# Kernel tuning notes

Measured on AMD Instinct MI355X. Metric: run time of the kernel, lower is better.

The kernel has to match this reference:

```python
import jax, jax.numpy as jnp
import numpy as np

NVAR, B, C, H, W = 3, 4, 256, 64, 64
C1 = C // 2          # dat channels (nc)
C2 = C - C1
HEADS = 4
HC = C1 // HEADS     # head channels
STRIDE = 4
KS = 4
HK, WK = H // STRIDE, W // STRIDE
NS = HK * WK         # n_sample
RPE_H, RPE_W = 2 * H - 1, 2 * W - 1
NPAIR = 3


def _grid_sample(img, grid):
    # img [B,C,Hi,Wi]; grid [B,Hg,Wg,2] = (x,y) in [-1,1]; bilinear, align_corners=True, zero-pad
    Bn, Cn, Hi, Wi = img.shape
    x = (grid[..., 0] + 1.0) * 0.5 * (Wi - 1)
    y = (grid[..., 1] + 1.0) * 0.5 * (Hi - 1)
    x0 = jnp.floor(x)
    y0 = jnp.floor(y)
    wx = x - x0
    wy = y - y0
    x0i = x0.astype(jnp.int32)
    y0i = y0.astype(jnp.int32)
    imt = img.transpose(0, 2, 3, 1)  # [B,Hi,Wi,C]
    bidx = jnp.arange(Bn)[:, None, None]

    def corner(yi, xi, wgt):
        ok = ((xi >= 0) & (xi < Wi) & (yi >= 0) & (yi < Hi)).astype(img.dtype)
        val = imt[bidx, jnp.clip(yi, 0, Hi - 1), jnp.clip(xi, 0, Wi - 1)]  # [B,Hg,Wg,C]
        return val * (wgt * ok)[..., None]

    out = (corner(y0i, x0i, (1 - wx) * (1 - wy))
           + corner(y0i, x0i + 1, wx * (1 - wy))
           + corner(y0i + 1, x0i, (1 - wx) * wy)
           + corner(y0i + 1, x0i + 1, wx * wy))
    return out.transpose(0, 3, 1, 2)  # [B,C,Hg,Wg]


def _ref_points(hk, wk):
    # normalized sampling-grid reference points, (y,x) order
    ry = (jnp.linspace(0.5, hk - 0.5, hk) / (hk - 1.0)) * 2.0 - 1.0
    rx = (jnp.linspace(0.5, wk - 0.5, wk) / (wk - 1.0)) * 2.0 - 1.0
    return jnp.stack(jnp.meshgrid(ry, rx, indexing='ij'), axis=-1)  # [hk,wk,2]


def _q_grid(h, w):
    gy = (jnp.arange(h, dtype=jnp.float32) / (h - 1.0)) * 2.0 - 1.0
    gx = (jnp.arange(w, dtype=jnp.float32) / (w - 1.0)) * 2.0 - 1.0
    return jnp.stack(jnp.meshgrid(gy, gx, indexing='ij'), axis=-1).reshape(h * w, 2)


def _conv1x1(x, w, b=None):
    y = jnp.einsum('oc,bchw->bohw', w, x)
    return y if b is None else y + b[None, :, None, None]


def _dat_block(q_in, kv_in, pWq, pbq, pWk, pbk, pWv, pbv, pWo, pbo,
               pdw_w, pdw_b, pln_g, pln_b, ppw_w, prpe):
    Bn = q_in.shape[0]
    q = _conv1x1(q_in, pWq, pbq)  # [B,C1,H,W]
    # offset net: depthwise 4x4 stride-4 conv -> channel LN -> GELU -> 1x1 conv to 2
    off = jax.lax.conv_general_dilated(
        q, pdw_w, (STRIDE, STRIDE), 'VALID',
        dimension_numbers=('NCHW', 'OIHW', 'NCHW'),
        feature_group_count=C1) + pdw_b[None, :, None, None]  # [B,C1,HK,WK]
    mu = off.mean(axis=1, keepdims=True)
    var = ((off - mu) ** 2).mean(axis=1, keepdims=True)
    off = (off - mu) * jax.lax.rsqrt(var + 1e-5) * pln_g[None, :, None, None] + pln_b[None, :, None, None]
    off = jax.nn.gelu(off, approximate=False)
    offset = _conv1x1(off, ppw_w).transpose(0, 2, 3, 1)  # [B,HK,WK,2] (dy,dx)
    # offset_range_factor = -1 -> no tanh scaling, clamp pos into [-1,1]
    pos = jnp.clip(offset + _ref_points(HK, WK)[None], -1.0, 1.0)  # [B,HK,WK,2]
    xs = _grid_sample(kv_in, pos[..., ::-1])  # sample kv at deformed points -> [B,C1,HK,WK]
    k = _conv1x1(xs, pWk, pbk).reshape(Bn, HEADS, HC, NS)
    v = _conv1x1(xs, pWv, pbv).reshape(Bn, HEADS, HC, NS)
    qh = q.reshape(Bn, HEADS, HC, H * W)
    attn = jnp.einsum('bhcm,bhcn->bhmn', qh, k) * (HC ** -0.5)  # [B,h,HW,NS]
    # relative position bias sampled from rpe table
    disp = (_q_grid(H, W)[None, :, None, :] - pos.reshape(Bn, 1, NS, 2)) * 0.5  # [B,HW,NS,2]
    rpe_b = jnp.broadcast_to(prpe[None], (Bn, HEADS, RPE_H, RPE_W))
    bias = _grid_sample(rpe_b, disp[..., ::-1])  # [B,h,HW,NS]
    attn = jax.nn.softmax(attn + bias, axis=-1)
    out = jnp.einsum('bhmn,bhcn->bhcm', attn, v).reshape(Bn, C1, H, W)
    return _conv1x1(out, pWo, pbo)


def _forward(xs, params):
    results = []
    num = 0
    for i in range(NVAR):
        res = xs[i]
        for j in range(i):
            attn_out = _dat_block(xs[i][:, :C1], xs[j][:, :C1],
                                  *(p[num] for p in params))
            # torch: res -= -cat(zeros[:,:C2], attn)  => add attn on channels C2:
            res = res.at[:, C2:].add(attn_out)
            num += 1
        results.append(res)
    return jnp.stack(results)  # [NVAR,B,C,H,W]


def setup_inputs() -> dict:
    key = jax.random.key(0)
    ks = jax.random.split(key, 4)
    d = {}
    for n, k in zip(['x0', 'x1', 'x2'], jax.random.split(ks[0], 3)):
        d[n] = jax.random.normal(k, (B, C, H, W), jnp.float32)

    def w(k, shape, s=0.02):
        return jax.random.normal(k, shape, jnp.float32) * s

    kk = jax.random.split(ks[1], 8)
    d['Wq'] = w(kk[0], (NPAIR, C1, C1))
    d['bq'] = jnp.zeros((NPAIR, C1), jnp.float32)
    d['Wk'] = w(kk[1], (NPAIR, C1, C1))
    d['bk'] = jnp.zeros((NPAIR, C1), jnp.float32)
    d['Wv'] = w(kk[2], (NPAIR, C1, C1))
    d['bv'] = jnp.zeros((NPAIR, C1), jnp.float32)
    d['Wo'] = w(kk[3], (NPAIR, C1, C1))
    d['bo'] = jnp.zeros((NPAIR, C1), jnp.float32)
    d['dw_w'] = w(kk[4], (NPAIR, C1, 1, KS, KS), 0.1)
    d['dw_b'] = jnp.zeros((NPAIR, C1), jnp.float32)
    d['ln_g'] = jnp.ones((NPAIR, C1), jnp.float32)
    d['ln_b'] = jnp.zeros((NPAIR, C1), jnp.float32)
    d['pw_w'] = w(kk[5], (NPAIR, 2, C1), 0.1)
    d['rpe'] = w(kk[6], (NPAIR, HEADS, RPE_H, RPE_W), 0.01)
    return d


def reference(x0, x1, x2, Wq, bq, Wk, bk, Wv, bv, Wo, bo,
              dw_w, dw_b, ln_g, ln_b, pw_w, rpe):
    params = (Wq, bq, Wk, bk, Wv, bv, Wo, bo, dw_w, dw_b, ln_g, ln_b, pw_w, rpe)
    out = _forward([x0, x1, x2], params)
    flow = jnp.zeros((NVAR, x0.shape[0]), out.dtype)
    return out, flow
```

## Files before the change

kernel.cpp:

```cpp
#include <hip/hip_runtime.h>
#include <math.h>

#define NVAR 3
#define BB 4
#define CC 256
#define C1 128
#define HEADS 4
#define HH 64
#define WW 64
#define HW 4096
#define RPE_W 127
#define NP 3
#define SCALE 0.17677669529663687f

typedef short bf16x8 __attribute__((ext_vector_type(8)));
typedef float f32x4 __attribute__((ext_vector_type(4)));
typedef __bf16 bf16x2 __attribute__((ext_vector_type(2)));

__device__ __forceinline__ unsigned short f2bf(float f) {
    unsigned int u = __float_as_uint(f);
    u += 0x7fffu + ((u >> 16) & 1u);
    return (unsigned short)(u >> 16);
}
__device__ __forceinline__ float bflo(unsigned u) { return __uint_as_float(u << 16); }
__device__ __forceinline__ float bfhi(unsigned u) { return __uint_as_float(u & 0xffff0000u); }

__device__ __forceinline__ float dot2bf(unsigned a, unsigned b, float c) {
#if __has_builtin(__builtin_amdgcn_fdot2_f32_bf16)
    return __builtin_amdgcn_fdot2_f32_bf16(__builtin_bit_cast(bf16x2, a),
                                           __builtin_bit_cast(bf16x2, b), c, false);
#else
    return c + bflo(a) * bflo(b) + bfhi(a) * bfhi(b);
#endif
}

__global__ __launch_bounds__(256) void prep_copy(const float* __restrict__ rpe,
                                                 const float* __restrict__ Wq,
                                                 const float* __restrict__ Wo,
                                                 const float* __restrict__ Wk,
                                                 const float* __restrict__ Wv,
                                                 const float* __restrict__ x0,
                                                 unsigned short* __restrict__ tabbf,
                                                 unsigned short* __restrict__ wqh,
                                                 unsigned short* __restrict__ wql,
                                                 unsigned short* __restrict__ woh,
                                                 unsigned short* __restrict__ wkh,
                                                 unsigned short* __restrict__ wvh,
                                                 float* __restrict__ out) {
    int blk = blockIdx.x;
    if (blk >= 24) {
        const long long n4 = (long long)BB * CC * HW / 4;
        long long i = (long long)(blk - 24) * 256 + threadIdx.x;
        const long long stride = 1024LL * 256;
        for (; i < n4 + 12; i += stride) {
            if (i < n4) ((float4*)out)[i] = ((const float4*)x0)[i];
            else out[3LL * BB * CC * HW + (i - n4)] = 0.f;
        }
        return;
    }
    if (blk < 12) {
        const float* src = rpe + (long long)blk * RPE_W * RPE_W;
        unsigned short* dst = tabbf + (long long)blk * 16384;
        for (int idx = threadIdx.x; idx < 16384; idx += 256) {
            int y = idx >> 7, x = idx & 127;
            float v = (y < RPE_W && x < RPE_W) ? src[y * RPE_W + x] : 0.f;
            dst[idx] = f2bf(v);
        }
    } else if (blk < 15) {
        int p = blk - 12;
        for (int i = threadIdx.x; i < 16384; i += 256) {
            float w = Wq[p * 16384 + i];
            unsigned short h = f2bf(w);
            wqh[p * 16384 + i] = h;
            wql[p * 16384 + i] = f2bf(w - bflo((unsigned)h));
        }
    } else if (blk < 18) {
        int p = blk - 15;
        for (int i = threadIdx.x; i < 16384; i += 256)
            woh[p * 16384 + i] = f2bf(Wo[p * 16384 + i]);
    } else if (blk < 21) {
        int p = blk - 18;
        for (int i = threadIdx.x; i < 16384; i += 256)
            wkh[p * 16384 + i] = f2bf(Wk[p * 16384 + i]);
    } else {
        int p = blk - 21;
        for (int i = threadIdx.x; i < 16384; i += 256)
            wvh[p * 16384 + i] = f2bf(Wv[p * 16384 + i]);
    }
}

__global__ __launch_bounds__(256) void conv_q(const float* __restrict__ x1,
                                              const float* __restrict__ x2,
                                              const unsigned short* __restrict__ wqh,
                                              const unsigned short* __restrict__ wql,
                                              const float* __restrict__ bq,
                                              float* __restrict__ qbuf,
                                              unsigned short* __restrict__ qbf,
                                              float* __restrict__ out) {
    __shared__ unsigned short qlds[4][16][136];
    int wid = threadIdx.x >> 6, lane = threadIdx.x & 63;
    int g = lane >> 4, lm = lane & 15;
    int gw = blockIdx.x * 4 + wid;
    int mt = gw & 255;
    int pb = gw >> 8;
    int p = pb >> 2, b = pb & 3;
    const float* X = ((p == 0) ? x1 : x2) + (long long)b * CC * HW;
    int m = mt * 16 + lm;
    float* outc = (p < 2)
        ? out + (((long long)((p + 1) * 4 + b)) * CC) * HW + m
        : nullptr;

    bf16x8 bhi[4], blo[4];
#pragma unroll
    for (int ksl = 0; ksl < 4; ksl++) {
        float v[8];
#pragma unroll
        for (int j = 0; j < 8; j++) {
            int k = ksl * 32 + 8 * g + j;
            v[j] = X[(long long)k * HW + m];
            if (outc) outc[(long long)k * HW] = v[j];
        }
        union { unsigned u[4]; bf16x8 v; } H, L;
#pragma unroll
        for (int t = 0; t < 4; t++) {
            unsigned short h0 = f2bf(v[2 * t]), h1 = f2bf(v[2 * t + 1]);
            unsigned short l0 = f2bf(v[2 * t] - bflo((unsigned)h0));
            unsigned short l1 = f2bf(v[2 * t + 1] - bflo((unsigned)h1));
            H.u[t] = (unsigned)h0 | ((unsigned)h1 << 16);
            L.u[t] = (unsigned)l0 | ((unsigned)l1 << 16);
        }
        bhi[ksl] = H.v;
        blo[ksl] = L.v;
    }

    const unsigned short* WH = wqh + p * 16384;
    const unsigned short* WL = wql + p * 16384;
    unsigned short* ql = &qlds[wid][lm][0];
    f32x4 zero = {0.f, 0.f, 0.f, 0.f};
#pragma unroll
    for (int ct2 = 0; ct2 < 4; ct2++) {
        int ct0 = 2 * ct2, ct1 = ct0 + 1;
        f32x4 a0 = zero, a1 = zero;
#pragma unroll
        for (int ksl = 0; ksl < 4; ksl++) {
            bf16x8 Ah0 = *(const bf16x8*)(WH + (ct0 * 16 + lm) * 128 + ksl * 32 + 8 * g);
            bf16x8 Al0 = *(const bf16x8*)(WL + (ct0 * 16 + lm) * 128 + ksl * 32 + 8 * g);
            bf16x8 Ah1 = *(const bf16x8*)(WH + (ct1 * 16 + lm) * 128 + ksl * 32 + 8 * g);
            bf16x8 Al1 = *(const bf16x8*)(WL + (ct1 * 16 + lm) * 128 + ksl * 32 + 8 * g);
            a0 = __builtin_amdgcn_mfma_f32_16x16x32_bf16(Ah0, bhi[ksl], a0, 0, 0, 0);
            a1 = __builtin_amdgcn_mfma_f32_16x16x32_bf16(Ah1, bhi[ksl], a1, 0, 0, 0);
            a0 = __builtin_amdgcn_mfma_f32_16x16x32_bf16(Ah0, blo[ksl], a0, 0, 0, 0);
            a1 = __builtin_amdgcn_mfma_f32_16x16x32_bf16(Ah1, blo[ksl], a1, 0, 0, 0);
            a0 = __builtin_amdgcn_mfma_f32_16x16x32_bf16(Al0, bhi[ksl], a0, 0, 0, 0);
            a1 = __builtin_amdgcn_mfma_f32_16x16x32_bf16(Al1, bhi[ksl], a1, 0, 0, 0);
        }
        float q0[4], q1[4];
#pragma unroll
        for (int r = 0; r < 4; r++) {
            int c0 = ct0 * 16 + 4 * g + r, c1 = ct1 * 16 + 4 * g + r;
            q0[r] = a0[r] + bq[p * 128 + c0];
            q1[r] = a1[r] + bq[p * 128 + c1];
            qbuf[((long long)pb * 128 + c0) * HW + m] = q0[r];
            qbuf[((long long)pb * 128 + c1) * HW + m] = q1[r];
        }
        *(unsigned*)(ql + ct0 * 16 + 4 * g) =
            (unsigned)f2bf(q0[0] * SCALE) | ((unsigned)f2bf(q0[1] * SCALE) << 16);
        *(unsigned*)(ql + ct0 * 16 + 4 * g + 2) =
            (unsigned)f2bf(q0[2] * SCALE) | ((unsigned)f2bf(q0[3] * SCALE) << 16);
        *(unsigned*)(ql + ct1 * 16 + 4 * g) =
            (unsigned)f2bf(q1[0] * SCALE) | ((unsigned)f2bf(q1[1] * SCALE) << 16);
        *(unsigned*)(ql + ct1 * 16 + 4 * g + 2) =
            (unsigned)f2bf(q1[2] * SCALE) | ((unsigned)f2bf(q1[3] * SCALE) << 16);
    }

    unsigned short* Yb = qbf + ((long long)pb * HW + mt * 16) * 128;
    int q = lane >> 4, cg = lane & 15;
#pragma unroll
    for (int i = 0; i < 4; i++) {
        int row = i * 4 + q;
        uint4 vv = *(const uint4*)&qlds[wid][row][cg * 8];
        *(uint4*)(Yb + row * 128 + cg * 8) = vv;
    }
}

__global__ __launch_bounds__(256) void mid_kernel(const float* __restrict__ qbuf,
                                                  const float* __restrict__ dw_w,
                                                  const float* __restrict__ dw_b,
                                                  const float* __restrict__ ln_g,
                                                  const float* __restrict__ ln_b,
                                                  const float* __restrict__ pw_w,
                                                  const float* __restrict__ x0,
                                                  const float* __restrict__ x1,
                                                  float* __restrict__ posb,
                                                  uint4* __restrict__ prmb,
                                                  unsigned short* __restrict__ xT) {
    __shared__ float sm[32 * 4 * 65 + 16 * 128];
    int blk = blockIdx.x;
    int tid = threadIdx.x;
    if (blk < 192) {
        float (*ld)[4][65] = (float(*)[4][65])sm;
        float (*dwout)[128] = (float(*)[128])(sm + 32 * 4 * 65);
        int pb = blk >> 4, hk = blk & 15;
        int p = pb >> 2;
        for (int cq = 0; cq < 4; cq++) {
            int c32 = cq * 32;
            __syncthreads();
#pragma unroll
            for (int it = 0; it < 8; it++) {
                int i2 = tid + it * 256;
                int c = i2 >> 6, rem = i2 & 63;
                int y = rem >> 4, xq = rem & 15;
                float4 v = *(const float4*)(qbuf + ((long long)pb * 128 + c32 + c) * HW
                                            + (4 * hk + y) * 64 + xq * 4);
                ld[c][y][xq * 4 + 0] = v.x;
                ld[c][y][xq * 4 + 1] = v.y;
                ld[c][y][xq * 4 + 2] = v.z;
                ld[c][y][xq * 4 + 3] = v.w;
            }
            __syncthreads();
            int wk = tid >> 4;
#pragma unroll
            for (int oi = 0; oi < 2; oi++) {
                int c = (tid & 15) + oi * 16;
                const float* dwp = dw_w + (p * 128 + c32 + c) * 16;
                float acc = dw_b[p * 128 + c32 + c];
#pragma unroll
                for (int ky = 0; ky < 4; ky++)
#pragma unroll
                    for (int kx = 0; kx < 4; kx++)
                        acc += ld[c][ky][wk * 4 + kx] * dwp[ky * 4 + kx];
                dwout[wk][c32 + c] = acc;
            }
        }
        __syncthreads();
        int wid = tid >> 6, lane = tid & 63;
        for (int i = 0; i < 4; i++) {
            int wk = wid * 4 + i;
            int s = hk * 16 + wk;
            float a0 = dwout[wk][lane], a1 = dwout[wk][lane + 64];
            float s1 = a0 + a1;
#pragma unroll
            for (int o = 1; o < 64; o <<= 1) s1 += __shfl_xor(s1, o);
            float mu = s1 * (1.f / 128.f);
            float d0 = a0 - mu, d1 = a1 - mu;
            float v2 = d0 * d0 + d1 * d1;
#pragma unroll
            for (int o = 1; o < 64; o <<= 1) v2 += __shfl_xor(v2, o);
            float rs = rsqrtf(v2 * (1.f / 128.f) + 1e-5f);
            int c0 = lane, c1 = lane + 64;
            float y0 = d0 * rs * ln_g[p * 128 + c0] + ln_b[p * 128 + c0];
            float y1 = d1 * rs * ln_g[p * 128 + c1] + ln_b[p * 128 + c1];
            float g0 = 0.5f * y0 * (1.f + erff(y0 * 0.70710678118654752f));
            float g1 = 0.5f * y1 * (1.f + erff(y1 * 0.70710678118654752f));
            float o0 = pw_w[(p * 2 + 0) * 128 + c0] * g0
                     + pw_w[(p * 2 + 0) * 128 + c1] * g1;
            float o1 = pw_w[(p * 2 + 1) * 128 + c0] * g0
                     + pw_w[(p * 2 + 1) * 128 + c1] * g1;
#pragma unroll
            for (int o = 1; o < 64; o <<= 1) o0 += __shfl_xor(o0, o);
#pragma unroll
            for (int o = 1; o < 64; o <<= 1) o1 += __shfl_xor(o1, o);
            if (lane == 0) {
                int wk2 = s & 15;
                float refy = (hk + 0.5f) * (2.f / 15.f) - 1.f;
                float refx = (wk2 + 0.5f) * (2.f / 15.f) - 1.f;
                float py = fminf(fmaxf(o0 + refy, -1.f), 1.f);
                float px = fminf(fmaxf(o1 + refx, -1.f), 1.f);
                int pbn = pb * 256 + s;
                posb[pbn * 2 + 0] = py;
                posb[pbn * 2 + 1] = px;
                float cy = 31.5f * (1.f - py), cx = 31.5f * (1.f - px);
                float yf = floorf(cy), xf = floorf(cx);
                float wy = cy - yf, wx = cx - xf;
                int Y0 = (int)yf, X0 = (int)xf;
                uint4 v;
                v.x = (unsigned)f2bf((1.f - wy) * (1.f - wx))
                    | ((unsigned)f2bf((1.f - wy) * wx) << 16);
                v.y = (unsigned)f2bf(wy * (1.f - wx))
                    | ((unsigned)f2bf(wy * wx) << 16);
                v.z = (unsigned)((Y0 * 128 + X0) * 2);
                v.w = 0;
                prmb[pbn] = v;
            }
        }
    } else {
        float (*ld2)[65] = (float(*)[65])sm;
        int rem = blk - 192;
        int v = rem >> 10;
        int rem1 = rem & 1023;
        int b = rem1 >> 8;
        int rem2 = rem1 & 255;
        int ct = rem2 >> 6;
        int mt = rem2 & 63;
        const float* src = ((v == 0) ? x0 : x1) + (long long)b * CC * HW
                           + (long long)(ct * 32) * HW + mt * 64;
#pragma unroll
        for (int it = 0; it < 2; it++) {
            int c = tid >> 3, x4 = (tid & 7) + it * 8;
            float4 w = *(const float4*)(src + (long long)c * HW + x4 * 4);
            ld2[c][x4 * 4 + 0] = w.x;
            ld2[c][x4 * 4 + 1] = w.y;
            ld2[c][x4 * 4 + 2] = w.z;
            ld2[c][x4 * 4 + 3] = w.w;
        }
        __syncthreads();
        int m = tid >> 2, cg = tid & 3;
        union { unsigned u[4]; } pk;
#pragma unroll
        for (int t = 0; t < 4; t++) {
            unsigned short h0 = f2bf(ld2[cg * 8 + 2 * t][m]);
            unsigned short h1 = f2bf(ld2[cg * 8 + 2 * t + 1][m]);
            pk.u[t] = (unsigned)h0 | ((unsigned)h1 << 16);
        }
        *(uint4*)(xT + (((long long)(v * 4 + b)) * HW + mt * 64 + m) * 128
                  + ct * 32 + cg * 8) = *(uint4*)pk.u;
    }
}

__global__ __launch_bounds__(256) void sample_kv(const unsigned short* __restrict__ xT,
                                                 const float* __restrict__ posb,
                                                 const unsigned short* __restrict__ wkh,
                                                 const unsigned short* __restrict__ wvh,
                                                 const float* __restrict__ bk,
                                                 const float* __restrict__ bv,
                                                 unsigned short* __restrict__ kbf,
                                                 unsigned short* __restrict__ vbf) {
    __shared__ unsigned short xls[32 * 128];
    int blk = blockIdx.x;
    int pb = blk >> 3;
    int nt = blk & 7;
    int p = pb >> 2, b = pb & 3;
    int n0 = nt * 32;
    int tid = threadIdx.x;

    {
        int nl = tid >> 3, co = tid & 7;
        int n = n0 + nl;
        float py = posb[(pb * 256 + n) * 2 + 0];
        float px = posb[(pb * 256 + n) * 2 + 1];
        float yi = (py + 1.f) * 31.5f, xi = (px + 1.f) * 31.5f;
        yi = fminf(fmaxf(yi, 0.f), 63.f);
        xi = fminf(fmaxf(xi, 0.f), 63.f);
        int y0 = min((int)yi, 62);
        int x0i = min((int)xi, 62);
        float wy = yi - (float)y0, wx = xi - (float)x0i;
        float w00 = (1.f - wy) * (1.f - wx), w01 = (1.f - wy) * wx;
        float w10 = wy * (1.f - wx), w11 = wy * wx;
        int vsel = (p == 2) ? 1 : 0;
        const unsigned short* base = xT + ((long long)(vsel * 4 + b)) * HW * 128;
        int m00 = y0 * 64 + x0i;
        char* dst = (char*)xls;
#pragma unroll
        for (int cb = 0; cb < 2; cb++) {
            int c0 = co * 16 + cb * 8;
            bf16x8 a = *(const bf16x8*)(base + (long long)m00 * 128 + c0);
            bf16x8 bb = *(const bf16x8*)(base + (long long)(m00 + 1) * 128 + c0);
            bf16x8 cc = *(const bf16x8*)(base + (long long)(m00 + 64) * 128 + c0);
            bf16x8 dd = *(const bf16x8*)(base + (long long)(m00 + 65) * 128 + c0);
            union { unsigned u[4]; bf16x8 v; } R;
#pragma unroll
            for (int t = 0; t < 4; t++) {
                float r0 = w00 * bflo((unsigned)(unsigned short)a[2 * t])
                         + w01 * bflo((unsigned)(unsigned short)bb[2 * t])
                         + w10 * bflo((unsigned)(unsigned short)cc[2 * t])
                         + w11 * bflo((unsigned)(unsigned short)dd[2 * t]);
                float r1 = w00 * bflo((unsigned)(unsigned short)a[2 * t + 1])
                         + w01 * bflo((unsigned)(unsigned short)bb[2 * t + 1])
                         + w10 * bflo((unsigned)(unsigned short)cc[2 * t + 1])
                         + w11 * bflo((unsigned)(unsigned short)dd[2 * t + 1]);
                R.u[t] = (unsigned)f2bf(r0) | ((unsigned)f2bf(r1) << 16);
            }
            *(bf16x8*)(dst + ((nl * 256 + c0 * 2) ^ ((nl & 7) << 4))) = R.v;
        }
    }
    __syncthreads();

    int wid = tid >> 6, lane = tid & 63;
    int g = lane >> 4, lm = lane & 15;
    int ntile = wid & 1, isv = wid >> 1;
    int nl = ntile * 16 + lm;
    const char* srcl = (const char*)xls;
    bf16x8 xf[4];
#pragma unroll
    for (int ks = 0; ks < 4; ks++)
        xf[ks] = *(const bf16x8*)(srcl + ((nl * 256 + (ks * 32 + 8 * g) * 2)
                                          ^ ((nl & 7) << 4)));
    f32x4 zero = {0.f, 0.f, 0.f, 0.f};
    if (!isv) {
        const unsigned short* WK = wkh + p * 16384;
#pragma unroll
        for (int ct = 0; ct < 8; ct++) {
            f32x4 acc = zero;
#pragma unroll
            for (int ks = 0; ks < 4; ks++) {
                bf16x8 wf = *(const bf16x8*)(WK + (ct * 16 + lm) * 128 + ks * 32 + 8 * g);
                acc = __builtin_amdgcn_mfma_f32_16x16x32_bf16(xf[ks], wf, acc, 0, 0, 0);
            }
            float bias = bk[p * 128 + ct * 16 + lm];
#pragma unroll
            for (int r = 0; r < 4; r++) {
                int n = n0 + ntile * 16 + 4 * g + r;
                kbf[((long long)pb * 256 + n) * 128 + ct * 16 + lm] = f2bf(acc[r] + bias);
            }
        }
    } else {
        const unsigned short* WV = wvh + p * 16384;
#pragma unroll
        for (int ct = 0; ct < 8; ct++) {
            f32x4 acc = zero;
#pragma unroll
            for (int ks = 0; ks < 4; ks++) {
                bf16x8 wf = *(const bf16x8*)(WV + (ct * 16 + lm) * 128 + ks * 32 + 8 * g);
                acc = __builtin_amdgcn_mfma_f32_16x16x32_bf16(wf, xf[ks], acc, 0, 0, 0);
            }
#pragma unroll
            for (int r = 0; r < 4; r++) {
                int c = ct * 16 + 4 * g + r;
                vbf[((long long)pb * 128 + c) * 256 + n0 + ntile * 16 + lm]
                    = f2bf(acc[r] + bv[p * 128 + c]);
            }
        }
    }
}

__global__ __launch_bounds__(512, 4) void attn_mfma(
        const unsigned short* __restrict__ qbf,
        const unsigned short* __restrict__ kbf,
        const unsigned short* __restrict__ vbf,
        const unsigned short* __restrict__ tabbf,
        const uint4* __restrict__ prmb,
        float* __restrict__ obuf) {
    __shared__ unsigned short tab[16384 + 8];
    __shared__ uint4 prm[256];
    int tid = threadIdx.x;
    int wid = tid >> 6, lane = tid & 63;
    int g = lane >> 4, lm = lane & 15;
    int bid = blockIdx.x;
    int my = ((bid & 31) << 1) + (wid >> 2);
    int h = (bid >> 5) & 3;
    int b = (bid >> 7) & 3;
    int p = bid >> 9;
    int pb = p * 4 + b;

    {
        const uint4* ts = (const uint4*)(tabbf + (long long)(p * 4 + h) * 16384);
        uint4* td = (uint4*)tab;
#pragma unroll
        for (int i = 0; i < 4; i++) td[tid + i * 512] = ts[tid + i * 512];
        if (tid < 256) prm[tid] = prmb[pb * 256 + tid];
    }
    __syncthreads();

    int mx = ((wid & 3) << 4) + lm;

    bf16x8 qf = *(const bf16x8*)(qbf + ((long long)pb * HW + my * 64 + mx) * 128
                                 + h * 32 + 8 * g);
    const unsigned short* kbase = kbf + ((long long)pb * 256 + lm) * 128
                                  + h * 32 + 8 * g;
    f32x4 zero = {0.f, 0.f, 0.f, 0.f};
    f32x4 acc[16];
    __builtin_amdgcn_s_setprio(1);
#pragma unroll
    for (int ni = 0; ni < 16; ni++) {
        bf16x8 kf = *(const bf16x8*)(kbase + ni * 16 * 128);
        acc[ni] = __builtin_amdgcn_mfma_f32_16x16x32_bf16(kf, qf, zero, 0, 0, 0);
    }
    __builtin_amdgcn_s_setprio(0);

    int laneoff = (my * 128 + mx) * 2;
    const char* tb = (const char*)tab;
#pragma unroll
    for (int ni = 0; ni < 16; ni++) {
#pragma unroll
        for (int r = 0; r < 4; r++) {
            int n = ni * 16 + 4 * g + r;
            uint4 pw = prm[n];
            int va = (int)pw.z + laneoff;
            int va4 = va & ~3;
            int sh = va & 3;
            unsigned r0 = *(const unsigned*)(tb + va4);
            unsigned r1 = *(const unsigned*)(tb + va4 + 4);
            unsigned r2 = *(const unsigned*)(tb + va4 + 256);
            unsigned r3 = *(const unsigned*)(tb + va4 + 260);
            unsigned p0 = __builtin_amdgcn_alignbyte(r1, r0, sh);
            unsigned p1 = __builtin_amdgcn_alignbyte(r3, r2, sh);
            float t = acc[ni][r];
            t = dot2bf(p0, pw.x, t);
            t = dot2bf(p1, pw.y, t);
            acc[ni][r] = t;
        }
    }

    float mxv = -1e30f;
#pragma unroll
    for (int ni = 0; ni < 16; ni++)
        mxv = fmaxf(mxv, fmaxf(fmaxf(acc[ni][0], acc[ni][1]),
                               fmaxf(acc[ni][2], acc[ni][3])));
    mxv = fmaxf(mxv, __shfl_xor(mxv, 16));
    mxv = fmaxf(mxv, __shfl_xor(mxv, 32));
    float sum = 0.f;
    unsigned dwA[16], dwB[16];
#pragma unroll
    for (int ni = 0; ni < 16; ni++) {
        float e0 = __expf(acc[ni][0] - mxv);
        float e1 = __expf(acc[ni][1] - mxv);
        float e2 = __expf(acc[ni][2] - mxv);
        float e3 = __expf(acc[ni][3] - mxv);
        sum += (e0 + e1) + (e2 + e3);
        asm("v_cvt_pk_bf16_f32 %0, %1, %2" : "=v"(dwA[ni]) : "v"(e0), "v"(e1));
        asm("v_cvt_pk_bf16_f32 %0, %1, %2" : "=v"(dwB[ni]) : "v"(e2), "v"(e3));
    }
    sum += __shfl_xor(sum, 16);
    sum += __shfl_xor(sum, 32);

    int src0 = ((g & 1) << 5) + lm;
    int src1 = src0 + 16;
    bool sel = (g >> 1) != 0;
    const unsigned short* vb0 = vbf + ((long long)pb * 128 + h * 32 + lm) * 256
                                + 8 * g;
    f32x4 o0 = zero, o1 = zero;
#pragma unroll
    for (int st = 0; st < 8; st++) {
        unsigned d0a = __shfl(dwA[2 * st], src0), d0b = __shfl(dwA[2 * st + 1], src0);
        unsigned d1a = __shfl(dwB[2 * st], src0), d1b = __shfl(dwB[2 * st + 1], src0);
        unsigned d2a = __shfl(dwA[2 * st], src1), d2b = __shfl(dwA[2 * st + 1], src1);
        unsigned d3a = __shfl(dwB[2 * st], src1), d3b = __shfl(dwB[2 * st + 1], src1);
        union { unsigned u[4]; bf16x8 v; } pf;
        pf.u[0] = sel ? d0b : d0a;
        pf.u[1] = sel ? d1b : d1a;
        pf.u[2] = sel ? d2b : d2a;
        pf.u[3] = sel ? d3b : d3a;
        bf16x8 v0 = *(const bf16x8*)(vb0 + st * 32);
        bf16x8 v1 = *(const bf16x8*)(vb0 + 4096 + st * 32);
        __builtin_amdgcn_s_setprio(1);
        o0 = __builtin_amdgcn_mfma_f32_16x16x32_bf16(v0, pf.v, o0, 0, 0, 0);
        o1 = __builtin_amdgcn_mfma_f32_16x16x32_bf16(v1, pf.v, o1, 0, 0, 0);
        __builtin_amdgcn_s_setprio(0);
    }

    float inv = 1.f / sum;
    float* ob = obuf + ((long long)pb * 128 + h * 32) * HW + my * 64 + mx;
#pragma unroll
    for (int r = 0; r < 4; r++) {
        ob[(g * 4 + r) * HW] = o0[r] * inv;
        ob[(16 + g * 4 + r) * HW] = o1[r] * inv;
    }
}

__global__ __launch_bounds__(256) void conv_wo(const float* __restrict__ x1,
                                               const float* __restrict__ x2,
                                               const float* __restrict__ obuf,
                                               const unsigned short* __restrict__ woh,
                                               const float* __restrict__ bo,
                                               float* __restrict__ out) {
    int wid = threadIdx.x >> 6, lane = threadIdx.x & 63;
    int g = lane >> 4, lm = lane & 15;
    int gw = blockIdx.x * 4 + wid;
    int mt = gw & 255;
    int b = (gw >> 8) & 3;
    int vs = gw >> 10;
    int m = mt * 16 + lm;
    int np = vs + 1;

    f32x4 acc[8];
#pragma unroll
    for (int ct = 0; ct < 8; ct++) acc[ct] = (f32x4){0.f, 0.f, 0.f, 0.f};

    for (int pi = 0; pi < np; pi++) {
        int p = vs ? (1 + pi) : 0;
        const float* O = obuf + (long long)(p * 4 + b) * 128 * HW;
        bf16x8 bh[4];
#pragma unroll
        for (int ksl = 0; ksl < 4; ksl++) {
            float v[8];
#pragma unroll
            for (int j = 0; j < 8; j++)
                v[j] = O[(long long)(ksl * 32 + 8 * g + j) * HW + m];
            union { unsigned u[4]; bf16x8 v; } H;
#pragma unroll
            for (int t = 0; t < 4; t++)
                H.u[t] = (unsigned)f2bf(v[2 * t]) | ((unsigned)f2bf(v[2 * t + 1]) << 16);
            bh[ksl] = H.v;
        }
        const unsigned short* WH = woh + p * 16384;
#pragma unroll
        for (int ct = 0; ct < 8; ct++)
#pragma unroll
            for (int ksl = 0; ksl < 4; ksl++) {
                bf16x8 A = *(const bf16x8*)(WH + (ct * 16 + lm) * 128 + ksl * 32 + 8 * g);
                acc[ct] = __builtin_amdgcn_mfma_f32_16x16x32_bf16(A, bh[ksl], acc[ct], 0, 0, 0);
            }
    }

    int qi = vs + 1;
    const float* xq = (vs ? x2 : x1) + (long long)b * CC * HW;
#pragma unroll
    for (int ct = 0; ct < 8; ct++)
#pragma unroll
        for (int r = 0; r < 4; r++) {
            int c = ct * 16 + 4 * g + r;
            float bias = vs ? (bo[128 + c] + bo[256 + c]) : bo[c];
            float base = xq[(long long)(128 + c) * HW + m];
            out[(((long long)(qi * 4 + b)) * CC + 128 + c) * HW + m]
                = base + acc[ct][r] + bias;
        }
}

extern "C" void kernel_launch(void* const* d_in, const int* in_sizes, int n_in,
                              void* d_out, int out_size, void* d_ws, size_t ws_size,
                              hipStream_t stream) {
    const float* x0 = (const float*)d_in[0];
    const float* x1 = (const float*)d_in[1];
    const float* x2 = (const float*)d_in[2];
    const float* Wq = (const float*)d_in[3];
    const float* bq = (const float*)d_in[4];
    const float* Wk = (const float*)d_in[5];
    const float* bk = (const float*)d_in[6];
    const float* Wv = (const float*)d_in[7];
    const float* bv = (const float*)d_in[8];
    const float* Wo = (const float*)d_in[9];
    const float* bo = (const float*)d_in[10];
    const float* dw_w = (const float*)d_in[11];
    const float* dw_b = (const float*)d_in[12];
    const float* ln_g = (const float*)d_in[13];
    const float* ln_b = (const float*)d_in[14];
    const float* pw_w = (const float*)d_in[15];
    const float* rpe = (const float*)d_in[16];
    float* out = (float*)d_out;

    float* ws = (float*)d_ws;
    float* qbuf = ws;
    float* obuf = qbuf;
    float* posb = ws + 6291456;
    unsigned short* xT = (unsigned short*)(posb + 6144);
    unsigned short* qbf = xT + 4194304;
    unsigned short* kbf = qbf + 12582912;
    unsigned short* vbf = kbf + 393216;
    unsigned short* tabbf = vbf + 393216;
    uint4* prmb = (uint4*)(tabbf + 196608);
    unsigned short* wqh = (unsigned short*)(prmb + 3072);
    unsigned short* wql = wqh + 49152;
    unsigned short* woh = wql + 49152;
    unsigned short* wkh = woh + 49152;
    unsigned short* wvh = wkh + 49152;

    prep_copy<<<1048, 256, 0, stream>>>(rpe, Wq, Wo, Wk, Wv, x0, tabbf,
                                        wqh, wql, woh, wkh, wvh, out);
    conv_q<<<768, 256, 0, stream>>>(x1, x2, wqh, wql, bq, qbuf, qbf, out);
    mid_kernel<<<2240, 256, 0, stream>>>(qbuf, dw_w, dw_b, ln_g, ln_b, pw_w,
                                         x0, x1, posb, prmb, xT);
    sample_kv<<<96, 256, 0, stream>>>(xT, posb, wkh, wvh, bk, bv, kbf, vbf);
    attn_mfma<<<1536, 512, 0, stream>>>(qbf, kbf, vbf, tabbf, prmb, obuf);
    conv_wo<<<512, 256, 0, stream>>>(x1, x2, obuf, woh, bo, out);
}
```

Measured before the change: 181.1 us.

## Use online softmax over two key chunks and read RPE table from global

```diff
diff --git a/kernel.cpp b/kernel.cpp
--- a/kernel.cpp
+++ b/kernel.cpp
@@ -423,122 +423,130 @@
     }
 }
 
-__global__ __launch_bounds__(512, 4) void attn_mfma(
+__global__ __launch_bounds__(256, 4) void attn_mfma(
         const unsigned short* __restrict__ qbf,
         const unsigned short* __restrict__ kbf,
         const unsigned short* __restrict__ vbf,
         const unsigned short* __restrict__ tabbf,
         const uint4* __restrict__ prmb,
         float* __restrict__ obuf) {
-    __shared__ unsigned short tab[16384 + 8];
     __shared__ uint4 prm[256];
     int tid = threadIdx.x;
     int wid = tid >> 6, lane = tid & 63;
     int g = lane >> 4, lm = lane & 15;
     int bid = blockIdx.x;
-    int my = ((bid & 31) << 1) + (wid >> 2);
-    int h = (bid >> 5) & 3;
-    int b = (bid >> 7) & 3;
-    int p = bid >> 9;
+    int my = bid & 63;
+    int h = (bid >> 6) & 3;
+    int b = (bid >> 8) & 3;
+    int p = bid >> 10;
     int pb = p * 4 + b;
 
-    {
-        const uint4* ts = (const uint4*)(tabbf + (long long)(p * 4 + h) * 16384);
-        uint4* td = (uint4*)tab;
-#pragma unroll
-        for (int i = 0; i < 4; i++) td[tid + i * 512] = ts[tid + i * 512];
-        if (tid < 256) prm[tid] = prmb[pb * 256 + tid];
-    }
+    prm[tid] = prmb[pb * 256 + tid];
     __syncthreads();
 
-    int mx = ((wid & 3) << 4) + lm;
+    int mx = (wid << 4) + lm;
 
     bf16x8 qf = *(const bf16x8*)(qbf + ((long long)pb * HW + my * 64 + mx) * 128
                                  + h * 32 + 8 * g);
     const unsigned short* kbase = kbf + ((long long)pb * 256 + lm) * 128
                                   + h * 32 + 8 * g;
+    const char* tbg = (const char*)(tabbf + (long long)(p * 4 + h) * 16384);
+    const unsigned short* vb0 = vbf + ((long long)pb * 128 + h * 32 + lm) * 256
+                                + 8 * g;
+    int laneoff = (my * 128 + mx) * 2;
+
     f32x4 zero = {0.f, 0.f, 0.f, 0.f};
-    f32x4 acc[16];
-    __builtin_amdgcn_s_setprio(1);
-#pragma unroll
-    for (int ni = 0; ni < 16; ni++) {
-        bf16x8 kf = *(const bf16x8*)(kbase + ni * 16 * 128);
-        acc[ni] = __builtin_amdgcn_mfma_f32_16x16x32_bf16(kf, qf, zero, 0, 0, 0);
-    }
-    __builtin_amdgcn_s_setprio(0);
-
-    int laneoff = (my * 128 + mx) * 2;
-    const char* tb = (const char*)tab;
-#pragma unroll
-    for (int ni = 0; ni < 16; ni++) {
-#pragma unroll
-        for (int r = 0; r < 4; r++) {
-            int n = ni * 16 + 4 * g + r;
-            uint4 pw = prm[n];
-            int va = (int)pw.z + laneoff;
-            int va4 = va & ~3;
-            int sh = va & 3;
-            unsigned r0 = *(const unsigned*)(tb + va4);
-            unsigned r1 = *(const unsigned*)(tb + va4 + 4);
-            unsigned r2 = *(const unsigned*)(tb + va4 + 256);
-            unsigned r3 = *(const unsigned*)(tb + va4 + 260);
-            unsigned p0 = __builtin_amdgcn_alignbyte(r1, r0, sh);
-            unsigned p1 = __builtin_amdgcn_alignbyte(r3, r2, sh);
-            float t = acc[ni][r];
-            t = dot2bf(p0, pw.x, t);
-            t = dot2bf(p1, pw.y, t);
-            acc[ni][r] = t;
-        }
-    }
-
-    float mxv = -1e30f;
-#pragma unroll
-    for (int ni = 0; ni < 16; ni++)
-        mxv = fmaxf(mxv, fmaxf(fmaxf(acc[ni][0], acc[ni][1]),
-                               fmaxf(acc[ni][2], acc[ni][3])));
-    mxv = fmaxf(mxv, __shfl_xor(mxv, 16));
-    mxv = fmaxf(mxv, __shfl_xor(mxv, 32));
-    float sum = 0.f;
-    unsigned dwA[16], dwB[16];
-#pragma unroll
-    for (int ni = 0; ni < 16; ni++) {
-        float e0 = __expf(acc[ni][0] - mxv);
-        float e1 = __expf(acc[ni][1] - mxv);
-        float e2 = __expf(acc[ni][2] - mxv);
-        float e3 = __expf(acc[ni][3] - mxv);
-        sum += (e0 + e1) + (e2 + e3);
-        asm("v_cvt_pk_bf16_f32 %0, %1, %2" : "=v"(dwA[ni]) : "v"(e0), "v"(e1));
-        asm("v_cvt_pk_bf16_f32 %0, %1, %2" : "=v"(dwB[ni]) : "v"(e2), "v"(e3));
-    }
-    sum += __shfl_xor(sum, 16);
-    sum += __shfl_xor(sum, 32);
-
+    f32x4 o0 = zero, o1 = zero;
+    float m_run = -1e30f, l_run = 0.f;
     int src0 = ((g & 1) << 5) + lm;
     int src1 = src0 + 16;
     bool sel = (g >> 1) != 0;
-    const unsigned short* vb0 = vbf + ((long long)pb * 128 + h * 32 + lm) * 256
-                                + 8 * g;
-    f32x4 o0 = zero, o1 = zero;
-#pragma unroll
-    for (int st = 0; st < 8; st++) {
-        unsigned d0a = __shfl(dwA[2 * st], src0), d0b = __shfl(dwA[2 * st + 1], src0);
-        unsigned d1a = __shfl(dwB[2 * st], src0), d1b = __shfl(dwB[2 * st + 1], src0);
-        unsigned d2a = __shfl(dwA[2 * st], src1), d2b = __shfl(dwA[2 * st + 1], src1);
-        unsigned d3a = __shfl(dwB[2 * st], src1), d3b = __shfl(dwB[2 * st + 1], src1);
-        union { unsigned u[4]; bf16x8 v; } pf;
-        pf.u[0] = sel ? d0b : d0a;
-        pf.u[1] = sel ? d1b : d1a;
-        pf.u[2] = sel ? d2b : d2a;
-        pf.u[3] = sel ? d3b : d3a;
-        bf16x8 v0 = *(const bf16x8*)(vb0 + st * 32);
-        bf16x8 v1 = *(const bf16x8*)(vb0 + 4096 + st * 32);
+
+#pragma unroll
+    for (int ch = 0; ch < 2; ch++) {
+        int nb = ch * 128;
+        f32x4 acc[8];
         __builtin_amdgcn_s_setprio(1);
-        o0 = __builtin_amdgcn_mfma_f32_16x16x32_bf16(v0, pf.v, o0, 0, 0, 0);
-        o1 = __builtin_amdgcn_mfma_f32_16x16x32_bf16(v1, pf.v, o1, 0, 0, 0);
+#pragma unroll
+        for (int ni = 0; ni < 8; ni++) {
+            bf16x8 kf = *(const bf16x8*)(kbase + (nb + ni * 16) * 128);
+            acc[ni] = __builtin_amdgcn_mfma_f32_16x16x32_bf16(kf, qf, zero, 0, 0, 0);
+        }
         __builtin_amdgcn_s_setprio(0);
-    }
-
-    float inv = 1.f / sum;
+
+#pragma unroll
+        for (int ni = 0; ni < 8; ni++) {
+#pragma unroll
+            for (int r = 0; r < 4; r++) {
+                int n = nb + ni * 16 + 4 * g + r;
+                uint4 pw = prm[n];
+                int va = (int)pw.z + laneoff;
+                int va4 = va & ~3;
+                int sh = va & 3;
+                unsigned r0 = *(const unsigned*)(tbg + va4);
+                unsigned r1 = *(const unsigned*)(tbg + va4 + 4);
+                unsigned r2 = *(const unsigned*)(tbg + va4 + 256);
+                unsigned r3 = *(const unsigned*)(tbg + va4 + 260);
+                unsigned p0 = __builtin_amdgcn_alignbyte(r1, r0, sh);
+                unsigned p1 = __builtin_amdgcn_alignbyte(r3, r2, sh);
+                float t = acc[ni][r];
+                t = dot2bf(p0, pw.x, t);
+                t = dot2bf(p1, pw.y, t);
+                acc[ni][r] = t;
+            }
+        }
+
+        float cmax = -1e30f;
+#pragma unroll
+        for (int ni = 0; ni < 8; ni++)
+            cmax = fmaxf(cmax, fmaxf(fmaxf(acc[ni][0], acc[ni][1]),
+                                     fmaxf(acc[ni][2], acc[ni][3])));
+        cmax = fmaxf(cmax, __shfl_xor(cmax, 16));
+        cmax = fmaxf(cmax, __shfl_xor(cmax, 32));
+        float m_new = fmaxf(m_run, cmax);
+        float scale = __expf(m_run - m_new);
+        l_run *= scale;
+#pragma unroll
+        for (int r = 0; r < 4; r++) { o0[r] *= scale; o1[r] *= scale; }
+        m_run = m_new;
+
+        float lsum = 0.f;
+        unsigned dwA[8], dwB[8];
+#pragma unroll
+        for (int ni = 0; ni < 8; ni++) {
+            float e0 = __expf(acc[ni][0] - m_run);
+            float e1 = __expf(acc[ni][1] - m_run);
+            float e2 = __expf(acc[ni][2] - m_run);
+            float e3 = __expf(acc[ni][3] - m_run);
+            lsum += (e0 + e1) + (e2 + e3);
+            asm("v_cvt_pk_bf16_f32 %0, %1, %2" : "=v"(dwA[ni]) : "v"(e0), "v"(e1));
+            asm("v_cvt_pk_bf16_f32 %0, %1, %2" : "=v"(dwB[ni]) : "v"(e2), "v"(e3));
+        }
+        lsum += __shfl_xor(lsum, 16);
+        lsum += __shfl_xor(lsum, 32);
+        l_run += lsum;
+
+#pragma unroll
+        for (int st = 0; st < 4; st++) {
+            unsigned d0a = __shfl(dwA[2 * st], src0), d0b = __shfl(dwA[2 * st + 1], src0);
+            unsigned d1a = __shfl(dwB[2 * st], src0), d1b = __shfl(dwB[2 * st + 1], src0);
+            unsigned d2a = __shfl(dwA[2 * st], src1), d2b = __shfl(dwA[2 * st + 1], src1);
+            unsigned d3a = __shfl(dwB[2 * st], src1), d3b = __shfl(dwB[2 * st + 1], src1);
+            union { unsigned u[4]; bf16x8 v; } pf;
+            pf.u[0] = sel ? d0b : d0a;
+            pf.u[1] = sel ? d1b : d1a;
+            pf.u[2] = sel ? d2b : d2a;
+            pf.u[3] = sel ? d3b : d3a;
+            bf16x8 v0 = *(const bf16x8*)(vb0 + nb + st * 32);
+            bf16x8 v1 = *(const bf16x8*)(vb0 + 4096 + nb + st * 32);
+            __builtin_amdgcn_s_setprio(1);
+            o0 = __builtin_amdgcn_mfma_f32_16x16x32_bf16(v0, pf.v, o0, 0, 0, 0);
+            o1 = __builtin_amdgcn_mfma_f32_16x16x32_bf16(v1, pf.v, o1, 0, 0, 0);
+            __builtin_amdgcn_s_setprio(0);
+        }
+    }
+
+    float inv = 1.f / l_run;
     float* ob = obuf + ((long long)pb * 128 + h * 32) * HW + my * 64 + mx;
 #pragma unroll
     for (int r = 0; r < 4; r++) {
@@ -650,6 +658,6 @@
     mid_kernel<<<2240, 256, 0, stream>>>(qbuf, dw_w, dw_b, ln_g, ln_b, pw_w,
                                          x0, x1, posb, prmb, xT);
     sample_kv<<<96, 256, 0, stream>>>(xT, posb, wkh, wvh, bk, bv, kbf, vbf);
-    attn_mfma<<<1536, 512, 0, stream>>>(qbf, kbf, vbf, tabbf, prmb, obuf);
+    attn_mfma<<<3072, 256, 0, stream>>>(qbf, kbf, vbf, tabbf, prmb, obuf);
     conv_wo<<<512, 256, 0, stream>>>(x1, x2, obuf, woh, bo, out);
 }
```

Measured after the change: 213.8 us (median of 2 runs). 1.18x slower.
